# Kernel tuning notes

Hardware: AMD Instinct MI355X
Metric: run time of the kernel (lower is better)

Reference implementation:

```python
import jax, jax.numpy as jnp
import numpy as np

B, K, IN, CH, M, N = 1024, 64, 128, 256, 4, 16


def setup_inputs() -> dict:
    key = jax.random.key(0)
    ks = jax.random.split(key, 12)
    s = 0.02
    return {
        "user_node": jax.random.normal(ks[0], (B, K, IN), jnp.float32),
        "RIS_node": jax.random.normal(ks[1], (B, IN), jnp.float32),
        "cas_channel": jax.random.normal(ks[2], (B, K, 2 * M * N), jnp.float32),
        "d_link": jax.random.normal(ks[3], (B, K, 2 * M), jnp.float32),
        # f2_user: Linear(3*IN -> CH), ReLU, Linear(CH -> CH)
        "W1": jax.random.normal(ks[4], (3 * IN, CH), jnp.float32) * s,
        "b1": jnp.zeros((CH,), jnp.float32),
        "W2": jax.random.normal(ks[5], (CH, CH), jnp.float32) * s,
        "b2": jnp.zeros((CH,), jnp.float32),
        # f3_RIS: Linear(2*IN -> CH), ReLU, Linear(CH -> CH)
        "W3": jax.random.normal(ks[6], (2 * IN, CH), jnp.float32) * s,
        "b3": jnp.zeros((CH,), jnp.float32),
        "W4": jax.random.normal(ks[7], (CH, CH), jnp.float32) * s,
        "b4": jnp.zeros((CH,), jnp.float32),
    }


def _leave_one_out_max(x):
    # x: (B, K, D). Exact leave-one-out max via prefix/suffix cummax, O(K).
    prefix = jax.lax.cummax(x, axis=1)                      # max over 0..k
    suffix = jax.lax.cummax(x[:, ::-1], axis=1)[:, ::-1]    # max over k..K-1
    neg = jnp.full_like(x[:, :1], -jnp.inf)
    left = jnp.concatenate([neg, prefix[:, :-1]], axis=1)   # max over 0..k-1
    right = jnp.concatenate([suffix[:, 1:], neg], axis=1)   # max over k+1..K-1
    return jnp.maximum(left, right)


def reference(user_node, RIS_node, cas_channel, d_link,
              W1, b1, W2, b2, W3, b3, W4, b4):
    b, k, d = user_node.shape
    mean_user = jnp.mean(user_node, axis=1)                 # (B, IN)
    loo_max = _leave_one_out_max(user_node)                 # (B, K, IN)
    ris_b = jnp.broadcast_to(RIS_node[:, None, :], (b, k, d))
    feat = jnp.concatenate([user_node, loo_max, ris_b], axis=-1)  # (B, K, 3*IN)
    h_user = jax.nn.relu(feat @ W1 + b1) @ W2 + b2          # (B, K, CH)
    user_node_update = jnp.concatenate([user_node, h_user], axis=-1)  # (B,K,IN+CH)
    rfeat = jnp.concatenate([RIS_node, mean_user], axis=-1)  # (B, 2*IN)
    h_ris = jax.nn.relu(rfeat @ W3 + b3) @ W4 + b4          # (B, CH)
    RIS_node_update = jnp.concatenate([RIS_node, h_ris], axis=-1)    # (B, IN+CH)
    return user_node_update, RIS_node_update
```

## Files before the change

### kernel.cpp

```cpp
#include <hip/hip_runtime.h>

typedef __attribute__((ext_vector_type(8))) short short8;
typedef __attribute__((ext_vector_type(4))) float f32x4;
typedef __attribute__((ext_vector_type(2))) unsigned u32x2;

__device__ __forceinline__ unsigned short f2bf(float f) {
  unsigned u = __builtin_bit_cast(unsigned, f);
  u += 0x7fffu + ((u >> 16) & 1u);
  return (unsigned short)(u >> 16);
}
__device__ __forceinline__ float bf2f(unsigned short u) {
  return __builtin_bit_cast(float, (unsigned)u << 16);
}
__device__ __forceinline__ unsigned pkbf(float a, float b) {
  unsigned r;
  asm("v_cvt_pk_bf16_f32 %0, %1, %2" : "=v"(r) : "v"(a), "v"(b));
  return r;
}

__global__ __launch_bounds__(256) void wprep(
    const float* __restrict__ W1, const float* __restrict__ W2,
    const float* __restrict__ W3, const float* __restrict__ W4,
    unsigned short* __restrict__ W1f, unsigned short* __restrict__ W2f,
    unsigned short* __restrict__ W3f, unsigned short* __restrict__ W4f) {
  int idx = (blockIdx.x * 256 + threadIdx.x) * 4;
  const float* src; unsigned short* dst; int kb; int rel;
  if (idx < 98304)        { src = W1; dst = W1f; kb = 12; rel = idx; }
  else if (idx < 163840)  { src = W2; dst = W2f; kb = 8;  rel = idx - 98304; }
  else if (idx < 229376)  { src = W3; dst = W3f; kb = 8;  rel = idx - 163840; }
  else                    { src = W4; dst = W4f; kb = 8;  rel = idx - 229376; }
  int kk = rel >> 8, n0 = rel & 255;
  f32x4 t = *(const f32x4*)(src + rel);
  #pragma unroll
  for (int j = 0; j < 4; ++j) {
    int n = n0 + j;
    int lane = (n & 15) | (((kk >> 3) & 3) << 4);
    int di = (((n >> 4) * kb + (kk >> 5)) * 64 + lane) * 8 + (kk & 7);
    dst[di] = f2bf(t[j]);
  }
}

__global__ __launch_bounds__(512, 4) void fusedU(
    const float* __restrict__ user, const float* __restrict__ ris,
    const unsigned short* __restrict__ W1f, const unsigned short* __restrict__ W2f,
    const float* __restrict__ b1, const float* __restrict__ b2,
    float* __restrict__ out0, unsigned short* __restrict__ meanb) {
  __shared__ __align__(16) unsigned short smem[16896];
  unsigned short* const U    = smem;
  unsigned short* const Hb   = smem;
  unsigned short* const m1s  = smem + 16384;
  unsigned short* const m2s  = smem + 16512;
  unsigned short* const ams  = smem + 16640;
  unsigned short* const risl = smem + 16768;

  const int tid = threadIdx.x;
  const int bx = blockIdx.x;
  const size_t ubase = (size_t)bx * 8192;

  #pragma unroll
  for (int it = 0; it < 4; ++it) {
    int e = it * 2048 + tid * 4;
    f32x4 t = *(const f32x4*)(user + ubase + e);
    int row = e >> 7, col = e & 127;
    *(f32x4*)(out0 + (size_t)(bx * 64 + row) * 384 + col) = t;
    u32x2 p = { pkbf(t[0], t[1]), pkbf(t[2], t[3]) };
    int cc = col >> 3, sub = col & 7;
    *(u32x2*)(U + row * 128 + ((cc ^ (row & 7)) << 3) + sub) = p;
  }
  if (tid < 128) risl[tid] = f2bf(ris[bx * 128 + tid]);
  __syncthreads();

  const int lane = tid & 63, wn = tid >> 6;
  const int r = lane & 15;
  const int k8 = (lane >> 4) * 8;
  const int j4 = (lane >> 4) * 4;

  if (tid < 128) {
    int c = tid;
    int cc = c >> 3, sub = c & 7;
    float m1 = -3.402823466e38f, m2 = -3.402823466e38f, s = 0.f;
    int amx = 0;
    #pragma unroll 8
    for (int row = 0; row < 64; ++row) {
      float v = bf2f(U[row * 128 + ((cc ^ (row & 7)) << 3) + sub]);
      s += v;
      if (v > m1) { m2 = m1; m1 = v; amx = row; }
      else if (v > m2) { m2 = v; }
    }
    m1s[c] = f2bf(m1); m2s[c] = f2bf(m2); ams[c] = (unsigned short)amx;
    meanb[bx * 128 + c] = f2bf(s * (1.f / 64.f));
  }

  f32x4 acc[4][2];
  #pragma unroll
  for (int a = 0; a < 4; ++a) { acc[a][0] = (f32x4)0.f; acc[a][1] = (f32x4)0.f; }

  #pragma unroll
  for (int fs = 0; fs < 4; ++fs) {
    short8 af[4];
    #pragma unroll
    for (int mf = 0; mf < 4; ++mf) {
      int row = mf * 16 + r;
      int cc = fs * 4 + (lane >> 4);
      af[mf] = *(const short8*)(U + row * 128 + ((cc ^ (row & 7)) << 3));
    }
    short8 w0 = *(const short8*)&W1f[(size_t)(((wn * 2 + 0) * 12 + fs) * 64 + lane) * 8];
    short8 w1 = *(const short8*)&W1f[(size_t)(((wn * 2 + 1) * 12 + fs) * 64 + lane) * 8];
    #pragma unroll
    for (int mf = 0; mf < 4; ++mf) {
      acc[mf][0] = __builtin_amdgcn_mfma_f32_16x16x32_bf16(af[mf], w0, acc[mf][0], 0, 0, 0);
      acc[mf][1] = __builtin_amdgcn_mfma_f32_16x16x32_bf16(af[mf], w1, acc[mf][1], 0, 0, 0);
    }
  }
  #pragma unroll
  for (int fs = 0; fs < 4; ++fs) {
    short8 v = *(const short8*)(risl + fs * 32 + k8);
    short8 w0 = *(const short8*)&W1f[(size_t)(((wn * 2 + 0) * 12 + 8 + fs) * 64 + lane) * 8];
    short8 w1 = *(const short8*)&W1f[(size_t)(((wn * 2 + 1) * 12 + 8 + fs) * 64 + lane) * 8];
    #pragma unroll
    for (int mf = 0; mf < 4; ++mf) {
      acc[mf][0] = __builtin_amdgcn_mfma_f32_16x16x32_bf16(v, w0, acc[mf][0], 0, 0, 0);
      acc[mf][1] = __builtin_amdgcn_mfma_f32_16x16x32_bf16(v, w1, acc[mf][1], 0, 0, 0);
    }
  }
  __syncthreads();

  #pragma unroll
  for (int fs = 0; fs < 4; ++fs) {
    int c0 = fs * 32 + k8;
    short8 m1v = *(const short8*)(m1s + c0);
    short8 m2v = *(const short8*)(m2s + c0);
    short8 amv = *(const short8*)(ams + c0);
    short8 w0 = *(const short8*)&W1f[(size_t)(((wn * 2 + 0) * 12 + 4 + fs) * 64 + lane) * 8];
    short8 w1 = *(const short8*)&W1f[(size_t)(((wn * 2 + 1) * 12 + 4 + fs) * 64 + lane) * 8];
    #pragma unroll
    for (int mf = 0; mf < 4; ++mf) {
      int rr = mf * 16 + r;
      short8 t;
      #pragma unroll
      for (int j = 0; j < 8; ++j)
        t[j] = ((unsigned short)amv[j] == (unsigned short)rr) ? m2v[j] : m1v[j];
      acc[mf][0] = __builtin_amdgcn_mfma_f32_16x16x32_bf16(t, w0, acc[mf][0], 0, 0, 0);
      acc[mf][1] = __builtin_amdgcn_mfma_f32_16x16x32_bf16(t, w1, acc[mf][1], 0, 0, 0);
    }
  }

  float ba[2] = { b1[wn * 32 + r], b1[wn * 32 + 16 + r] };
  #pragma unroll
  for (int mf = 0; mf < 4; ++mf)
    #pragma unroll
    for (int nf = 0; nf < 2; ++nf)
      #pragma unroll
      for (int j = 0; j < 4; ++j) {
        int rr = mf * 16 + j4 + j;
        int col = wn * 32 + nf * 16 + r;
        int cc = col >> 3;
        Hb[rr * 256 + ((cc ^ (rr & 7)) << 3) + (col & 7)] =
            f2bf(fmaxf(acc[mf][nf][j] + ba[nf], 0.f));
      }
  __syncthreads();

  f32x4 acc2[4][2];
  #pragma unroll
  for (int a = 0; a < 4; ++a) { acc2[a][0] = (f32x4)0.f; acc2[a][1] = (f32x4)0.f; }
  #pragma unroll
  for (int kc = 0; kc < 8; ++kc) {
    short8 af[4];
    #pragma unroll
    for (int mf = 0; mf < 4; ++mf) {
      int rr = mf * 16 + r;
      int cc = kc * 4 + (lane >> 4);
      af[mf] = *(const short8*)(Hb + rr * 256 + ((cc ^ (rr & 7)) << 3));
    }
    short8 w0 = *(const short8*)&W2f[(size_t)(((wn * 2 + 0) * 8 + kc) * 64 + lane) * 8];
    short8 w1 = *(const short8*)&W2f[(size_t)(((wn * 2 + 1) * 8 + kc) * 64 + lane) * 8];
    #pragma unroll
    for (int mf = 0; mf < 4; ++mf) {
      acc2[mf][0] = __builtin_amdgcn_mfma_f32_16x16x32_bf16(af[mf], w0, acc2[mf][0], 0, 0, 0);
      acc2[mf][1] = __builtin_amdgcn_mfma_f32_16x16x32_bf16(af[mf], w1, acc2[mf][1], 0, 0, 0);
    }
  }

  float bb[2] = { b2[wn * 32 + r], b2[wn * 32 + 16 + r] };
  #pragma unroll
  for (int mf = 0; mf < 4; ++mf)
    #pragma unroll
    for (int nf = 0; nf < 2; ++nf)
      #pragma unroll
      for (int j = 0; j < 4; ++j) {
        int rr = mf * 16 + j4 + j;
        int col = wn * 32 + nf * 16 + r;
        out0[(size_t)(bx * 64 + rr) * 384 + 128 + col] = acc2[mf][nf][j] + bb[nf];
      }
}

__global__ __launch_bounds__(512, 4) void fusedR(
    const float* __restrict__ ris, const unsigned short* __restrict__ meanb,
    const unsigned short* __restrict__ W3f, const unsigned short* __restrict__ W4f,
    const float* __restrict__ b3, const float* __restrict__ b4,
    float* __restrict__ out1) {
  __shared__ unsigned short Hb[64 * 256];

  const int tid = threadIdx.x;
  const int row0 = blockIdx.x * 64;

  #pragma unroll
  for (int it = 0; it < 4; ++it) {
    int e = it * 2048 + tid * 4;
    f32x4 t = *(const f32x4*)(ris + (size_t)row0 * 128 + e);
    int row = e >> 7, col = e & 127;
    *(f32x4*)(out1 + (size_t)(row0 + row) * 384 + col) = t;
  }

  const int lane = tid & 63, wn = tid >> 6;
  const int r = lane & 15;
  const int k8 = (lane >> 4) * 8;
  const int j4 = (lane >> 4) * 4;

  f32x4 acc[4][2];
  #pragma unroll
  for (int a = 0; a < 4; ++a) { acc[a][0] = (f32x4)0.f; acc[a][1] = (f32x4)0.f; }

  #pragma unroll
  for (int fs = 0; fs < 8; ++fs) {
    short8 af[4];
    if (fs < 4) {
      #pragma unroll
      for (int mf = 0; mf < 4; ++mf) {
        const float* p = &ris[(size_t)(row0 + mf * 16 + r) * 128 + fs * 32 + k8];
        f32x4 t0 = *(const f32x4*)p;
        f32x4 t1 = *(const f32x4*)(p + 4);
        short8 t;
        #pragma unroll
        for (int j = 0; j < 4; ++j) { t[j] = (short)f2bf(t0[j]); t[4 + j] = (short)f2bf(t1[j]); }
        af[mf] = t;
      }
    } else {
      #pragma unroll
      for (int mf = 0; mf < 4; ++mf)
        af[mf] = *(const short8*)&meanb[(size_t)(row0 + mf * 16 + r) * 128 + (fs - 4) * 32 + k8];
    }
    short8 w0 = *(const short8*)&W3f[(size_t)(((wn * 2 + 0) * 8 + fs) * 64 + lane) * 8];
    short8 w1 = *(const short8*)&W3f[(size_t)(((wn * 2 + 1) * 8 + fs) * 64 + lane) * 8];
    #pragma unroll
    for (int mf = 0; mf < 4; ++mf) {
      acc[mf][0] = __builtin_amdgcn_mfma_f32_16x16x32_bf16(af[mf], w0, acc[mf][0], 0, 0, 0);
      acc[mf][1] = __builtin_amdgcn_mfma_f32_16x16x32_bf16(af[mf], w1, acc[mf][1], 0, 0, 0);
    }
  }

  float ba[2] = { b3[wn * 32 + r], b3[wn * 32 + 16 + r] };
  #pragma unroll
  for (int mf = 0; mf < 4; ++mf)
    #pragma unroll
    for (int nf = 0; nf < 2; ++nf)
      #pragma unroll
      for (int j = 0; j < 4; ++j) {
        int rr = mf * 16 + j4 + j;
        int col = wn * 32 + nf * 16 + r;
        int cc = col >> 3;
        Hb[rr * 256 + ((cc ^ (rr & 7)) << 3) + (col & 7)] =
            f2bf(fmaxf(acc[mf][nf][j] + ba[nf], 0.f));
      }
  __syncthreads();

  f32x4 acc2[4][2];
  #pragma unroll
  for (int a = 0; a < 4; ++a) { acc2[a][0] = (f32x4)0.f; acc2[a][1] = (f32x4)0.f; }
  #pragma unroll
  for (int kc = 0; kc < 8; ++kc) {
    short8 af[4];
    #pragma unroll
    for (int mf = 0; mf < 4; ++mf) {
      int rr = mf * 16 + r;
      int cc = kc * 4 + (lane >> 4);
      af[mf] = *(const short8*)(Hb + rr * 256 + ((cc ^ (rr & 7)) << 3));
    }
    short8 w0 = *(const short8*)&W4f[(size_t)(((wn * 2 + 0) * 8 + kc) * 64 + lane) * 8];
    short8 w1 = *(const short8*)&W4f[(size_t)(((wn * 2 + 1) * 8 + kc) * 64 + lane) * 8];
    #pragma unroll
    for (int mf = 0; mf < 4; ++mf) {
      acc2[mf][0] = __builtin_amdgcn_mfma_f32_16x16x32_bf16(af[mf], w0, acc2[mf][0], 0, 0, 0);
      acc2[mf][1] = __builtin_amdgcn_mfma_f32_16x16x32_bf16(af[mf], w1, acc2[mf][1], 0, 0, 0);
    }
  }

  float bb[2] = { b4[wn * 32 + r], b4[wn * 32 + 16 + r] };
  #pragma unroll
  for (int mf = 0; mf < 4; ++mf)
    #pragma unroll
    for (int nf = 0; nf < 2; ++nf)
      #pragma unroll
      for (int j = 0; j < 4; ++j) {
        int rr = mf * 16 + j4 + j;
        int col = wn * 32 + nf * 16 + r;
        out1[(size_t)(row0 + rr) * 384 + 128 + col] = acc2[mf][nf][j] + bb[nf];
      }
}

extern "C" void kernel_launch(void* const* d_in, const int* in_sizes, int n_in,
                              void* d_out, int out_size, void* d_ws, size_t ws_size,
                              hipStream_t stream) {
  const float* user = (const float*)d_in[0];
  const float* ris  = (const float*)d_in[1];
  const float* W1 = (const float*)d_in[4];
  const float* b1 = (const float*)d_in[5];
  const float* W2 = (const float*)d_in[6];
  const float* b2 = (const float*)d_in[7];
  const float* W3 = (const float*)d_in[8];
  const float* b3 = (const float*)d_in[9];
  const float* W4 = (const float*)d_in[10];
  const float* b4 = (const float*)d_in[11];

  float* out0 = (float*)d_out;
  float* out1 = out0 + (size_t)65536 * 384;

  char* ws = (char*)d_ws;
  unsigned short* meanb = (unsigned short*)(ws);
  unsigned short* W1f   = (unsigned short*)(ws + 262144);
  unsigned short* W2f   = (unsigned short*)(ws + 458752);
  unsigned short* W3f   = (unsigned short*)(ws + 589824);
  unsigned short* W4f   = (unsigned short*)(ws + 720896);

  hipLaunchKernelGGL(wprep, dim3(288), dim3(256), 0, stream,
                     W1, W2, W3, W4, W1f, W2f, W3f, W4f);
  hipLaunchKernelGGL(fusedU, dim3(1024), dim3(512), 0, stream,
                     user, ris, W1f, W2f, b1, b2, out0, meanb);
  hipLaunchKernelGGL(fusedR, dim3(16), dim3(512), 0, stream,
                     ris, meanb, W3f, W4f, b3, b4, out1);
}
```

Before: 70.64 us.

## Split passthrough copy into extra blocks and prefetch weight fragments in batches

Adds 512 extra blocks to the main kernel that only copy user_node into the first 128 columns of out0, taking that strided store off the compute blocks. The compute blocks now load W1/W2 fragments in batches of four k-steps ahead of the MFMA loops so global latency overlaps, and the mean store moves to the end. Launch bounds drop from 4 to 2 waves per SIMD to make room for the extra registers, which lowers occupancy.

```diff
diff --git a/kernel.cpp b/kernel.cpp
--- a/kernel.cpp
+++ b/kernel.cpp
@@ -40,11 +40,23 @@
   }
 }
 
-__global__ __launch_bounds__(512, 4) void fusedU(
+__global__ __launch_bounds__(512, 2) void mega(
     const float* __restrict__ user, const float* __restrict__ ris,
     const unsigned short* __restrict__ W1f, const unsigned short* __restrict__ W2f,
     const float* __restrict__ b1, const float* __restrict__ b2,
     float* __restrict__ out0, unsigned short* __restrict__ meanb) {
+  if (blockIdx.x >= 1024) {
+    int cb = blockIdx.x - 1024;
+    #pragma unroll
+    for (int it = 0; it < 8; ++it) {
+      int g = cb * 4096 + it * 512 + threadIdx.x;
+      f32x4 t = *((const f32x4*)user + g);
+      int row = g >> 5, col = (g & 31) << 2;
+      *(f32x4*)(out0 + (size_t)row * 384 + col) = t;
+    }
+    return;
+  }
+
   __shared__ __align__(16) unsigned short smem[16896];
   unsigned short* const U    = smem;
   unsigned short* const Hb   = smem;
@@ -62,7 +74,6 @@
     int e = it * 2048 + tid * 4;
     f32x4 t = *(const f32x4*)(user + ubase + e);
     int row = e >> 7, col = e & 127;
-    *(f32x4*)(out0 + (size_t)(bx * 64 + row) * 384 + col) = t;
     u32x2 p = { pkbf(t[0], t[1]), pkbf(t[2], t[3]) };
     int cc = col >> 3, sub = col & 7;
     *(u32x2*)(U + row * 128 + ((cc ^ (row & 7)) << 3) + sub) = p;
@@ -75,53 +86,72 @@
   const int k8 = (lane >> 4) * 8;
   const int j4 = (lane >> 4) * 4;
 
+  float my_s = 0.f;
   if (tid < 128) {
-    int c = tid;
-    int cc = c >> 3, sub = c & 7;
-    float m1 = -3.402823466e38f, m2 = -3.402823466e38f, s = 0.f;
+    int c = tid, cc = c >> 3, sub = c & 7;
+    float m1 = -3.402823466e38f, m2 = -3.402823466e38f;
     int amx = 0;
     #pragma unroll 8
     for (int row = 0; row < 64; ++row) {
       float v = bf2f(U[row * 128 + ((cc ^ (row & 7)) << 3) + sub]);
-      s += v;
+      my_s += v;
       if (v > m1) { m2 = m1; m1 = v; amx = row; }
       else if (v > m2) { m2 = v; }
     }
     m1s[c] = f2bf(m1); m2s[c] = f2bf(m2); ams[c] = (unsigned short)amx;
-    meanb[bx * 128 + c] = f2bf(s * (1.f / 64.f));
   }
 
   f32x4 acc[4][2];
   #pragma unroll
   for (int a = 0; a < 4; ++a) { acc[a][0] = (f32x4)0.f; acc[a][1] = (f32x4)0.f; }
 
+  {
+    short8 wv[4][2];
+    #pragma unroll
+    for (int fs = 0; fs < 4; ++fs) {
+      wv[fs][0] = *(const short8*)&W1f[(size_t)(((wn * 2 + 0) * 12 + fs) * 64 + lane) * 8];
+      wv[fs][1] = *(const short8*)&W1f[(size_t)(((wn * 2 + 1) * 12 + fs) * 64 + lane) * 8];
+    }
+    #pragma unroll
+    for (int fs = 0; fs < 4; ++fs) {
+      short8 af[4];
+      #pragma unroll
+      for (int mf = 0; mf < 4; ++mf) {
+        int row = mf * 16 + r;
+        int cc = fs * 4 + (lane >> 4);
+        af[mf] = *(const short8*)(U + row * 128 + ((cc ^ (row & 7)) << 3));
+      }
+      #pragma unroll
+      for (int mf = 0; mf < 4; ++mf) {
+        acc[mf][0] = __builtin_amdgcn_mfma_f32_16x16x32_bf16(af[mf], wv[fs][0], acc[mf][0], 0, 0, 0);
+        acc[mf][1] = __builtin_amdgcn_mfma_f32_16x16x32_bf16(af[mf], wv[fs][1], acc[mf][1], 0, 0, 0);
+      }
+    }
+  }
+
+  {
+    short8 wv[4][2];
+    #pragma unroll
+    for (int fs = 0; fs < 4; ++fs) {
+      wv[fs][0] = *(const short8*)&W1f[(size_t)(((wn * 2 + 0) * 12 + 8 + fs) * 64 + lane) * 8];
+      wv[fs][1] = *(const short8*)&W1f[(size_t)(((wn * 2 + 1) * 12 + 8 + fs) * 64 + lane) * 8];
+    }
+    #pragma unroll
+    for (int fs = 0; fs < 4; ++fs) {
+      short8 v = *(const short8*)(risl + fs * 32 + k8);
+      #pragma unroll
+      for (int mf = 0; mf < 4; ++mf) {
+        acc[mf][0] = __builtin_amdgcn_mfma_f32_16x16x32_bf16(v, wv[fs][0], acc[mf][0], 0, 0, 0);
+        acc[mf][1] = __builtin_amdgcn_mfma_f32_16x16x32_bf16(v, wv[fs][1], acc[mf][1], 0, 0, 0);
+      }
+    }
+  }
+
+  short8 wvl[4][2];
   #pragma unroll
   for (int fs = 0; fs < 4; ++fs) {
-    short8 af[4];
-    #pragma unroll
-    for (int mf = 0; mf < 4; ++mf) {
-      int row = mf * 16 + r;
-      int cc = fs * 4 + (lane >> 4);
-      af[mf] = *(const short8*)(U + row * 128 + ((cc ^ (row & 7)) << 3));
-    }
-    short8 w0 = *(const short8*)&W1f[(size_t)(((wn * 2 + 0) * 12 + fs) * 64 + lane) * 8];
-    short8 w1 = *(const short8*)&W1f[(size_t)(((wn * 2 + 1) * 12 + fs) * 64 + lane) * 8];
-    #pragma unroll
-    for (int mf = 0; mf < 4; ++mf) {
-      acc[mf][0] = __builtin_amdgcn_mfma_f32_16x16x32_bf16(af[mf], w0, acc[mf][0], 0, 0, 0);
-      acc[mf][1] = __builtin_amdgcn_mfma_f32_16x16x32_bf16(af[mf], w1, acc[mf][1], 0, 0, 0);
-    }
-  }
-  #pragma unroll
-  for (int fs = 0; fs < 4; ++fs) {
-    short8 v = *(const short8*)(risl + fs * 32 + k8);
-    short8 w0 = *(const short8*)&W1f[(size_t)(((wn * 2 + 0) * 12 + 8 + fs) * 64 + lane) * 8];
-    short8 w1 = *(const short8*)&W1f[(size_t)(((wn * 2 + 1) * 12 + 8 + fs) * 64 + lane) * 8];
-    #pragma unroll
-    for (int mf = 0; mf < 4; ++mf) {
-      acc[mf][0] = __builtin_amdgcn_mfma_f32_16x16x32_bf16(v, w0, acc[mf][0], 0, 0, 0);
-      acc[mf][1] = __builtin_amdgcn_mfma_f32_16x16x32_bf16(v, w1, acc[mf][1], 0, 0, 0);
-    }
+    wvl[fs][0] = *(const short8*)&W1f[(size_t)(((wn * 2 + 0) * 12 + 4 + fs) * 64 + lane) * 8];
+    wvl[fs][1] = *(const short8*)&W1f[(size_t)(((wn * 2 + 1) * 12 + 4 + fs) * 64 + lane) * 8];
   }
   __syncthreads();
 
@@ -131,8 +161,6 @@
     short8 m1v = *(const short8*)(m1s + c0);
     short8 m2v = *(const short8*)(m2s + c0);
     short8 amv = *(const short8*)(ams + c0);
-    short8 w0 = *(const short8*)&W1f[(size_t)(((wn * 2 + 0) * 12 + 4 + fs) * 64 + lane) * 8];
-    short8 w1 = *(const short8*)&W1f[(size_t)(((wn * 2 + 1) * 12 + 4 + fs) * 64 + lane) * 8];
     #pragma unroll
     for (int mf = 0; mf < 4; ++mf) {
       int rr = mf * 16 + r;
@@ -140,8 +168,8 @@
       #pragma unroll
       for (int j = 0; j < 8; ++j)
         t[j] = ((unsigned short)amv[j] == (unsigned short)rr) ? m2v[j] : m1v[j];
-      acc[mf][0] = __builtin_amdgcn_mfma_f32_16x16x32_bf16(t, w0, acc[mf][0], 0, 0, 0);
-      acc[mf][1] = __builtin_amdgcn_mfma_f32_16x16x32_bf16(t, w1, acc[mf][1], 0, 0, 0);
+      acc[mf][0] = __builtin_amdgcn_mfma_f32_16x16x32_bf16(t, wvl[fs][0], acc[mf][0], 0, 0, 0);
+      acc[mf][1] = __builtin_amdgcn_mfma_f32_16x16x32_bf16(t, wvl[fs][1], acc[mf][1], 0, 0, 0);
     }
   }
 
@@ -158,13 +186,20 @@
         Hb[rr * 256 + ((cc ^ (rr & 7)) << 3) + (col & 7)] =
             f2bf(fmaxf(acc[mf][nf][j] + ba[nf], 0.f));
       }
+
+  short8 wv2[4][2];
+  #pragma unroll
+  for (int kc = 0; kc < 4; ++kc) {
+    wv2[kc][0] = *(const short8*)&W2f[(size_t)(((wn * 2 + 0) * 8 + kc) * 64 + lane) * 8];
+    wv2[kc][1] = *(const short8*)&W2f[(size_t)(((wn * 2 + 1) * 8 + kc) * 64 + lane) * 8];
+  }
   __syncthreads();
 
   f32x4 acc2[4][2];
   #pragma unroll
   for (int a = 0; a < 4; ++a) { acc2[a][0] = (f32x4)0.f; acc2[a][1] = (f32x4)0.f; }
   #pragma unroll
-  for (int kc = 0; kc < 8; ++kc) {
+  for (int kc = 0; kc < 4; ++kc) {
     short8 af[4];
     #pragma unroll
     for (int mf = 0; mf < 4; ++mf) {
@@ -172,12 +207,33 @@
       int cc = kc * 4 + (lane >> 4);
       af[mf] = *(const short8*)(Hb + rr * 256 + ((cc ^ (rr & 7)) << 3));
     }
-    short8 w0 = *(const short8*)&W2f[(size_t)(((wn * 2 + 0) * 8 + kc) * 64 + lane) * 8];
-    short8 w1 = *(const short8*)&W2f[(size_t)(((wn * 2 + 1) * 8 + kc) * 64 + lane) * 8];
-    #pragma unroll
-    for (int mf = 0; mf < 4; ++mf) {
-      acc2[mf][0] = __builtin_amdgcn_mfma_f32_16x16x32_bf16(af[mf], w0, acc2[mf][0], 0, 0, 0);
-      acc2[mf][1] = __builtin_amdgcn_mfma_f32_16x16x32_bf16(af[mf], w1, acc2[mf][1], 0, 0, 0);
+    #pragma unroll
+    for (int mf = 0; mf < 4; ++mf) {
+      acc2[mf][0] = __builtin_amdgcn_mfma_f32_16x16x32_bf16(af[mf], wv2[kc][0], acc2[mf][0], 0, 0, 0);
+      acc2[mf][1] = __builtin_amdgcn_mfma_f32_16x16x32_bf16(af[mf], wv2[kc][1], acc2[mf][1], 0, 0, 0);
+    }
+  }
+  {
+    short8 wv[4][2];
+    #pragma unroll
+    for (int kc = 0; kc < 4; ++kc) {
+      wv[kc][0] = *(const short8*)&W2f[(size_t)(((wn * 2 + 0) * 8 + 4 + kc) * 64 + lane) * 8];
+      wv[kc][1] = *(const short8*)&W2f[(size_t)(((wn * 2 + 1) * 8 + 4 + kc) * 64 + lane) * 8];
+    }
+    #pragma unroll
+    for (int kc = 0; kc < 4; ++kc) {
+      short8 af[4];
+      #pragma unroll
+      for (int mf = 0; mf < 4; ++mf) {
+        int rr = mf * 16 + r;
+        int cc = (4 + kc) * 4 + (lane >> 4);
+        af[mf] = *(const short8*)(Hb + rr * 256 + ((cc ^ (rr & 7)) << 3));
+      }
+      #pragma unroll
+      for (int mf = 0; mf < 4; ++mf) {
+        acc2[mf][0] = __builtin_amdgcn_mfma_f32_16x16x32_bf16(af[mf], wv[kc][0], acc2[mf][0], 0, 0, 0);
+        acc2[mf][1] = __builtin_amdgcn_mfma_f32_16x16x32_bf16(af[mf], wv[kc][1], acc2[mf][1], 0, 0, 0);
+      }
     }
   }
 
@@ -192,6 +248,8 @@
         int col = wn * 32 + nf * 16 + r;
         out0[(size_t)(bx * 64 + rr) * 384 + 128 + col] = acc2[mf][nf][j] + bb[nf];
       }
+
+  if (tid < 128) meanb[bx * 128 + tid] = f2bf(my_s * (1.f / 64.f));
 }
 
 __global__ __launch_bounds__(512, 4) void fusedR(
@@ -324,7 +382,7 @@
 
   hipLaunchKernelGGL(wprep, dim3(288), dim3(256), 0, stream,
                      W1, W2, W3, W4, W1f, W2f, W3f, W4f);
-  hipLaunchKernelGGL(fusedU, dim3(1024), dim3(512), 0, stream,
+  hipLaunchKernelGGL(mega, dim3(1536), dim3(512), 0, stream,
                      user, ris, W1f, W2f, b1, b2, out0, meanb);
   hipLaunchKernelGGL(fusedR, dim3(16), dim3(512), 0, stream,
                      ris, meanb, W3f, W4f, b3, b4, out1);
```

Measured after the change: 73.48 us. +4.0%, slower.

## Halve fusedU block to 4 waves with 64-column per-wave tiles and MFMA priority

Applied to the files above, without the earlier changes.

The fusedU kernel now runs 256 threads (4 waves) per block instead of 512. Each wave computes a 64x64 output tile (4x4 MFMA fragments) instead of 64x32, so each A fragment loaded from LDS is reused across four B fragments. s_setprio is raised around the MFMA bursts, and the mean store is moved to the end of the kernel. This raises accumulator register pressure (launch bounds 256,3) and halves the threads available for the copy and reduction phases.

```diff
diff --git a/kernel.cpp b/kernel.cpp
--- a/kernel.cpp
+++ b/kernel.cpp
@@ -40,7 +40,7 @@
   }
 }
 
-__global__ __launch_bounds__(512, 4) void fusedU(
+__global__ __launch_bounds__(256, 3) void fusedU(
     const float* __restrict__ user, const float* __restrict__ ris,
     const unsigned short* __restrict__ W1f, const unsigned short* __restrict__ W2f,
     const float* __restrict__ b1, const float* __restrict__ b2,
@@ -58,8 +58,8 @@
   const size_t ubase = (size_t)bx * 8192;
 
   #pragma unroll
-  for (int it = 0; it < 4; ++it) {
-    int e = it * 2048 + tid * 4;
+  for (int it = 0; it < 8; ++it) {
+    int e = it * 1024 + tid * 4;
     f32x4 t = *(const f32x4*)(user + ubase + e);
     int row = e >> 7, col = e & 127;
     *(f32x4*)(out0 + (size_t)(bx * 64 + row) * 384 + col) = t;
@@ -72,56 +72,66 @@
 
   const int lane = tid & 63, wn = tid >> 6;
   const int r = lane & 15;
-  const int k8 = (lane >> 4) * 8;
-  const int j4 = (lane >> 4) * 4;
-
+  const int g = lane >> 4;
+  const int k8 = g * 8;
+  const int j4 = g * 4;
+
+  float my_s = 0.f;
   if (tid < 128) {
-    int c = tid;
-    int cc = c >> 3, sub = c & 7;
-    float m1 = -3.402823466e38f, m2 = -3.402823466e38f, s = 0.f;
+    int c = tid, cc = c >> 3, sub = c & 7;
+    float m1 = -3.402823466e38f, m2 = -3.402823466e38f;
     int amx = 0;
     #pragma unroll 8
     for (int row = 0; row < 64; ++row) {
       float v = bf2f(U[row * 128 + ((cc ^ (row & 7)) << 3) + sub]);
-      s += v;
+      my_s += v;
       if (v > m1) { m2 = m1; m1 = v; amx = row; }
       else if (v > m2) { m2 = v; }
     }
     m1s[c] = f2bf(m1); m2s[c] = f2bf(m2); ams[c] = (unsigned short)amx;
-    meanb[bx * 128 + c] = f2bf(s * (1.f / 64.f));
-  }
-
-  f32x4 acc[4][2];
-  #pragma unroll
-  for (int a = 0; a < 4; ++a) { acc[a][0] = (f32x4)0.f; acc[a][1] = (f32x4)0.f; }
+  }
+
+  f32x4 acc[4][4];
+  #pragma unroll
+  for (int a = 0; a < 4; ++a)
+    #pragma unroll
+    for (int q = 0; q < 4; ++q) acc[a][q] = (f32x4)0.f;
 
   #pragma unroll
   for (int fs = 0; fs < 4; ++fs) {
-    short8 af[4];
+    short8 af[4], bf[4];
     #pragma unroll
     for (int mf = 0; mf < 4; ++mf) {
       int row = mf * 16 + r;
-      int cc = fs * 4 + (lane >> 4);
+      int cc = fs * 4 + g;
       af[mf] = *(const short8*)(U + row * 128 + ((cc ^ (row & 7)) << 3));
     }
-    short8 w0 = *(const short8*)&W1f[(size_t)(((wn * 2 + 0) * 12 + fs) * 64 + lane) * 8];
-    short8 w1 = *(const short8*)&W1f[(size_t)(((wn * 2 + 1) * 12 + fs) * 64 + lane) * 8];
-    #pragma unroll
-    for (int mf = 0; mf < 4; ++mf) {
-      acc[mf][0] = __builtin_amdgcn_mfma_f32_16x16x32_bf16(af[mf], w0, acc[mf][0], 0, 0, 0);
-      acc[mf][1] = __builtin_amdgcn_mfma_f32_16x16x32_bf16(af[mf], w1, acc[mf][1], 0, 0, 0);
-    }
-  }
+    #pragma unroll
+    for (int nf = 0; nf < 4; ++nf)
+      bf[nf] = *(const short8*)&W1f[(size_t)(((wn * 4 + nf) * 12 + fs) * 64 + lane) * 8];
+    __builtin_amdgcn_s_setprio(1);
+    #pragma unroll
+    for (int mf = 0; mf < 4; ++mf)
+      #pragma unroll
+      for (int nf = 0; nf < 4; ++nf)
+        acc[mf][nf] = __builtin_amdgcn_mfma_f32_16x16x32_bf16(af[mf], bf[nf], acc[mf][nf], 0, 0, 0);
+    __builtin_amdgcn_s_setprio(0);
+  }
+
   #pragma unroll
   for (int fs = 0; fs < 4; ++fs) {
     short8 v = *(const short8*)(risl + fs * 32 + k8);
-    short8 w0 = *(const short8*)&W1f[(size_t)(((wn * 2 + 0) * 12 + 8 + fs) * 64 + lane) * 8];
-    short8 w1 = *(const short8*)&W1f[(size_t)(((wn * 2 + 1) * 12 + 8 + fs) * 64 + lane) * 8];
-    #pragma unroll
-    for (int mf = 0; mf < 4; ++mf) {
-      acc[mf][0] = __builtin_amdgcn_mfma_f32_16x16x32_bf16(v, w0, acc[mf][0], 0, 0, 0);
-      acc[mf][1] = __builtin_amdgcn_mfma_f32_16x16x32_bf16(v, w1, acc[mf][1], 0, 0, 0);
-    }
+    short8 bf[4];
+    #pragma unroll
+    for (int nf = 0; nf < 4; ++nf)
+      bf[nf] = *(const short8*)&W1f[(size_t)(((wn * 4 + nf) * 12 + 8 + fs) * 64 + lane) * 8];
+    __builtin_amdgcn_s_setprio(1);
+    #pragma unroll
+    for (int mf = 0; mf < 4; ++mf)
+      #pragma unroll
+      for (int nf = 0; nf < 4; ++nf)
+        acc[mf][nf] = __builtin_amdgcn_mfma_f32_16x16x32_bf16(v, bf[nf], acc[mf][nf], 0, 0, 0);
+    __builtin_amdgcn_s_setprio(0);
   }
   __syncthreads();
 
@@ -131,8 +141,11 @@
     short8 m1v = *(const short8*)(m1s + c0);
     short8 m2v = *(const short8*)(m2s + c0);
     short8 amv = *(const short8*)(ams + c0);
-    short8 w0 = *(const short8*)&W1f[(size_t)(((wn * 2 + 0) * 12 + 4 + fs) * 64 + lane) * 8];
-    short8 w1 = *(const short8*)&W1f[(size_t)(((wn * 2 + 1) * 12 + 4 + fs) * 64 + lane) * 8];
+    short8 bf[4];
+    #pragma unroll
+    for (int nf = 0; nf < 4; ++nf)
+      bf[nf] = *(const short8*)&W1f[(size_t)(((wn * 4 + nf) * 12 + 4 + fs) * 64 + lane) * 8];
+    __builtin_amdgcn_s_setprio(1);
     #pragma unroll
     for (int mf = 0; mf < 4; ++mf) {
       int rr = mf * 16 + r;
@@ -140,58 +153,71 @@
       #pragma unroll
       for (int j = 0; j < 8; ++j)
         t[j] = ((unsigned short)amv[j] == (unsigned short)rr) ? m2v[j] : m1v[j];
-      acc[mf][0] = __builtin_amdgcn_mfma_f32_16x16x32_bf16(t, w0, acc[mf][0], 0, 0, 0);
-      acc[mf][1] = __builtin_amdgcn_mfma_f32_16x16x32_bf16(t, w1, acc[mf][1], 0, 0, 0);
-    }
-  }
-
-  float ba[2] = { b1[wn * 32 + r], b1[wn * 32 + 16 + r] };
+      #pragma unroll
+      for (int nf = 0; nf < 4; ++nf)
+        acc[mf][nf] = __builtin_amdgcn_mfma_f32_16x16x32_bf16(t, bf[nf], acc[mf][nf], 0, 0, 0);
+    }
+    __builtin_amdgcn_s_setprio(0);
+  }
+
+  float ba[4];
+  #pragma unroll
+  for (int nf = 0; nf < 4; ++nf) ba[nf] = b1[wn * 64 + nf * 16 + r];
   #pragma unroll
   for (int mf = 0; mf < 4; ++mf)
     #pragma unroll
-    for (int nf = 0; nf < 2; ++nf)
+    for (int nf = 0; nf < 4; ++nf)
       #pragma unroll
       for (int j = 0; j < 4; ++j) {
         int rr = mf * 16 + j4 + j;
-        int col = wn * 32 + nf * 16 + r;
+        int col = wn * 64 + nf * 16 + r;
         int cc = col >> 3;
         Hb[rr * 256 + ((cc ^ (rr & 7)) << 3) + (col & 7)] =
             f2bf(fmaxf(acc[mf][nf][j] + ba[nf], 0.f));
       }
   __syncthreads();
 
-  f32x4 acc2[4][2];
-  #pragma unroll
-  for (int a = 0; a < 4; ++a) { acc2[a][0] = (f32x4)0.f; acc2[a][1] = (f32x4)0.f; }
+  f32x4 acc2[4][4];
+  #pragma unroll
+  for (int a = 0; a < 4; ++a)
+    #pragma unroll
+    for (int q = 0; q < 4; ++q) acc2[a][q] = (f32x4)0.f;
   #pragma unroll
   for (int kc = 0; kc < 8; ++kc) {
-    short8 af[4];
+    short8 af[4], bf[4];
     #pragma unroll
     for (int mf = 0; mf < 4; ++mf) {
       int rr = mf * 16 + r;
-      int cc = kc * 4 + (lane >> 4);
+      int cc = kc * 4 + g;
       af[mf] = *(const short8*)(Hb + rr * 256 + ((cc ^ (rr & 7)) << 3));
     }
-    short8 w0 = *(const short8*)&W2f[(size_t)(((wn * 2 + 0) * 8 + kc) * 64 + lane) * 8];
-    short8 w1 = *(const short8*)&W2f[(size_t)(((wn * 2 + 1) * 8 + kc) * 64 + lane) * 8];
-    #pragma unroll
-    for (int mf = 0; mf < 4; ++mf) {
-      acc2[mf][0] = __builtin_amdgcn_mfma_f32_16x16x32_bf16(af[mf], w0, acc2[mf][0], 0, 0, 0);
-      acc2[mf][1] = __builtin_amdgcn_mfma_f32_16x16x32_bf16(af[mf], w1, acc2[mf][1], 0, 0, 0);
-    }
-  }
-
-  float bb[2] = { b2[wn * 32 + r], b2[wn * 32 + 16 + r] };
+    #pragma unroll
+    for (int nf = 0; nf < 4; ++nf)
+      bf[nf] = *(const short8*)&W2f[(size_t)(((wn * 4 + nf) * 8 + kc) * 64 + lane) * 8];
+    __builtin_amdgcn_s_setprio(1);
+    #pragma unroll
+    for (int mf = 0; mf < 4; ++mf)
+      #pragma unroll
+      for (int nf = 0; nf < 4; ++nf)
+        acc2[mf][nf] = __builtin_amdgcn_mfma_f32_16x16x32_bf16(af[mf], bf[nf], acc2[mf][nf], 0, 0, 0);
+    __builtin_amdgcn_s_setprio(0);
+  }
+
+  float bb[4];
+  #pragma unroll
+  for (int nf = 0; nf < 4; ++nf) bb[nf] = b2[wn * 64 + nf * 16 + r];
   #pragma unroll
   for (int mf = 0; mf < 4; ++mf)
     #pragma unroll
-    for (int nf = 0; nf < 2; ++nf)
+    for (int nf = 0; nf < 4; ++nf)
       #pragma unroll
       for (int j = 0; j < 4; ++j) {
         int rr = mf * 16 + j4 + j;
-        int col = wn * 32 + nf * 16 + r;
+        int col = wn * 64 + nf * 16 + r;
         out0[(size_t)(bx * 64 + rr) * 384 + 128 + col] = acc2[mf][nf][j] + bb[nf];
       }
+
+  if (tid < 128) meanb[bx * 128 + tid] = f2bf(my_s * (1.f / 64.f));
 }
 
 __global__ __launch_bounds__(512, 4) void fusedR(
@@ -324,7 +350,7 @@
 
   hipLaunchKernelGGL(wprep, dim3(288), dim3(256), 0, stream,
                      W1, W2, W3, W4, W1f, W2f, W3f, W4f);
-  hipLaunchKernelGGL(fusedU, dim3(1024), dim3(512), 0, stream,
+  hipLaunchKernelGGL(fusedU, dim3(1024), dim3(256), 0, stream,
                      user, ris, W1f, W2f, b1, b2, out0, meanb);
   hipLaunchKernelGGL(fusedR, dim3(16), dim3(512), 0, stream,
                      ris, meanb, W3f, W4f, b3, b4, out1);
```

Measured after the change: 73.17 us. 1.04x slower.

## Process two batch items per fusedU block to reuse weight fragments

Applied to the files above, without the earlier changes.

Each fusedU block now handles two batch items (128 rows) instead of one, so every W1/W2 fragment loaded from global memory feeds 8 MFMA row tiles instead of 4. The grid is halved, LDS per block doubles, and accumulators double, with launch bounds relaxed to one block per CU. The cost is higher register pressure and lower occupancy, which may reduce latency hiding, plus fewer blocks for load balancing across CUs.

```diff
diff --git a/kernel.cpp b/kernel.cpp
--- a/kernel.cpp
+++ b/kernel.cpp
@@ -40,85 +40,91 @@
   }
 }
 
-__global__ __launch_bounds__(512, 4) void fusedU(
+__global__ __launch_bounds__(512, 1) void fusedU(
     const float* __restrict__ user, const float* __restrict__ ris,
     const unsigned short* __restrict__ W1f, const unsigned short* __restrict__ W2f,
     const float* __restrict__ b1, const float* __restrict__ b2,
     float* __restrict__ out0, unsigned short* __restrict__ meanb) {
-  __shared__ __align__(16) unsigned short smem[16896];
+  __shared__ __align__(16) unsigned short smem[33792];
   unsigned short* const U    = smem;
   unsigned short* const Hb   = smem;
-  unsigned short* const m1s  = smem + 16384;
-  unsigned short* const m2s  = smem + 16512;
-  unsigned short* const ams  = smem + 16640;
-  unsigned short* const risl = smem + 16768;
+  unsigned short* const m1s  = smem + 32768;
+  unsigned short* const m2s  = smem + 33024;
+  unsigned short* const ams  = smem + 33280;
+  unsigned short* const risl = smem + 33536;
 
   const int tid = threadIdx.x;
   const int bx = blockIdx.x;
-  const size_t ubase = (size_t)bx * 8192;
-
-  #pragma unroll
-  for (int it = 0; it < 4; ++it) {
+  const size_t ubase = (size_t)bx * 16384;
+
+  #pragma unroll
+  for (int it = 0; it < 8; ++it) {
     int e = it * 2048 + tid * 4;
     f32x4 t = *(const f32x4*)(user + ubase + e);
     int row = e >> 7, col = e & 127;
-    *(f32x4*)(out0 + (size_t)(bx * 64 + row) * 384 + col) = t;
+    *(f32x4*)(out0 + (size_t)(bx * 128 + row) * 384 + col) = t;
     u32x2 p = { pkbf(t[0], t[1]), pkbf(t[2], t[3]) };
     int cc = col >> 3, sub = col & 7;
     *(u32x2*)(U + row * 128 + ((cc ^ (row & 7)) << 3) + sub) = p;
   }
-  if (tid < 128) risl[tid] = f2bf(ris[bx * 128 + tid]);
+  if (tid < 256) risl[tid] = f2bf(ris[bx * 256 + tid]);
   __syncthreads();
 
   const int lane = tid & 63, wn = tid >> 6;
-  const int r = lane & 15;
-  const int k8 = (lane >> 4) * 8;
-  const int j4 = (lane >> 4) * 4;
-
-  if (tid < 128) {
-    int c = tid;
+  const int r = lane & 15, g = lane >> 4;
+  const int k8 = g * 8;
+  const int j4 = g * 4;
+
+  float my_s = 0.f;
+  if (tid < 256) {
+    int bh = tid >> 7, c = tid & 127;
     int cc = c >> 3, sub = c & 7;
-    float m1 = -3.402823466e38f, m2 = -3.402823466e38f, s = 0.f;
+    float m1 = -3.402823466e38f, m2 = -3.402823466e38f;
     int amx = 0;
     #pragma unroll 8
     for (int row = 0; row < 64; ++row) {
-      float v = bf2f(U[row * 128 + ((cc ^ (row & 7)) << 3) + sub]);
-      s += v;
+      int gr = bh * 64 + row;
+      float v = bf2f(U[gr * 128 + ((cc ^ (gr & 7)) << 3) + sub]);
+      my_s += v;
       if (v > m1) { m2 = m1; m1 = v; amx = row; }
       else if (v > m2) { m2 = v; }
     }
-    m1s[c] = f2bf(m1); m2s[c] = f2bf(m2); ams[c] = (unsigned short)amx;
-    meanb[bx * 128 + c] = f2bf(s * (1.f / 64.f));
-  }
-
-  f32x4 acc[4][2];
-  #pragma unroll
-  for (int a = 0; a < 4; ++a) { acc[a][0] = (f32x4)0.f; acc[a][1] = (f32x4)0.f; }
+    m1s[bh * 128 + c] = f2bf(m1);
+    m2s[bh * 128 + c] = f2bf(m2);
+    ams[bh * 128 + c] = (unsigned short)amx;
+  }
+
+  f32x4 acc[8][2];
+  #pragma unroll
+  for (int a = 0; a < 8; ++a) { acc[a][0] = (f32x4)0.f; acc[a][1] = (f32x4)0.f; }
 
   #pragma unroll
   for (int fs = 0; fs < 4; ++fs) {
-    short8 af[4];
-    #pragma unroll
-    for (int mf = 0; mf < 4; ++mf) {
-      int row = mf * 16 + r;
-      int cc = fs * 4 + (lane >> 4);
-      af[mf] = *(const short8*)(U + row * 128 + ((cc ^ (row & 7)) << 3));
-    }
     short8 w0 = *(const short8*)&W1f[(size_t)(((wn * 2 + 0) * 12 + fs) * 64 + lane) * 8];
     short8 w1 = *(const short8*)&W1f[(size_t)(((wn * 2 + 1) * 12 + fs) * 64 + lane) * 8];
-    #pragma unroll
-    for (int mf = 0; mf < 4; ++mf) {
+    short8 af[8];
+    #pragma unroll
+    for (int mf = 0; mf < 8; ++mf) {
+      int row = mf * 16 + r;
+      int cc = fs * 4 + g;
+      af[mf] = *(const short8*)(U + row * 128 + ((cc ^ (row & 7)) << 3));
+    }
+    #pragma unroll
+    for (int mf = 0; mf < 8; ++mf) {
       acc[mf][0] = __builtin_amdgcn_mfma_f32_16x16x32_bf16(af[mf], w0, acc[mf][0], 0, 0, 0);
       acc[mf][1] = __builtin_amdgcn_mfma_f32_16x16x32_bf16(af[mf], w1, acc[mf][1], 0, 0, 0);
     }
   }
+
   #pragma unroll
   for (int fs = 0; fs < 4; ++fs) {
-    short8 v = *(const short8*)(risl + fs * 32 + k8);
     short8 w0 = *(const short8*)&W1f[(size_t)(((wn * 2 + 0) * 12 + 8 + fs) * 64 + lane) * 8];
     short8 w1 = *(const short8*)&W1f[(size_t)(((wn * 2 + 1) * 12 + 8 + fs) * 64 + lane) * 8];
-    #pragma unroll
-    for (int mf = 0; mf < 4; ++mf) {
+    short8 v0 = *(const short8*)(risl + fs * 32 + k8);
+    short8 v1 = *(const short8*)(risl + 128 + fs * 32 + k8);
+    #pragma unroll
+    for (int mf = 0; mf < 8; ++mf) {
+      const short8 v = (mf < 4) ? v0 : v1;
       acc[mf][0] = __builtin_amdgcn_mfma_f32_16x16x32_bf16(v, w0, acc[mf][0], 0, 0, 0);
       acc[mf][1] = __builtin_amdgcn_mfma_f32_16x16x32_bf16(v, w1, acc[mf][1], 0, 0, 0);
     }
@@ -127,19 +133,25 @@
 
   #pragma unroll
   for (int fs = 0; fs < 4; ++fs) {
-    int c0 = fs * 32 + k8;
-    short8 m1v = *(const short8*)(m1s + c0);
-    short8 m2v = *(const short8*)(m2s + c0);
-    short8 amv = *(const short8*)(ams + c0);
     short8 w0 = *(const short8*)&W1f[(size_t)(((wn * 2 + 0) * 12 + 4 + fs) * 64 + lane) * 8];
     short8 w1 = *(const short8*)&W1f[(size_t)(((wn * 2 + 1) * 12 + 4 + fs) * 64 + lane) * 8];
-    #pragma unroll
-    for (int mf = 0; mf < 4; ++mf) {
-      int rr = mf * 16 + r;
+    int c0 = fs * 32 + k8;
+    short8 m1a = *(const short8*)(m1s + c0);
+    short8 m2a = *(const short8*)(m2s + c0);
+    short8 ama = *(const short8*)(ams + c0);
+    short8 m1b_ = *(const short8*)(m1s + 128 + c0);
+    short8 m2b_ = *(const short8*)(m2s + 128 + c0);
+    short8 amb = *(const short8*)(ams + 128 + c0);
+    #pragma unroll
+    for (int mf = 0; mf < 8; ++mf) {
+      int rk = (mf * 16 + r) & 63;
+      const short8 m1v = (mf < 4) ? m1a : m1b_;
+      const short8 m2v = (mf < 4) ? m2a : m2b_;
+      const short8 amv = (mf < 4) ? ama : amb;
       short8 t;
       #pragma unroll
       for (int j = 0; j < 8; ++j)
-        t[j] = ((unsigned short)amv[j] == (unsigned short)rr) ? m2v[j] : m1v[j];
+        t[j] = ((unsigned short)amv[j] == (unsigned short)rk) ? m2v[j] : m1v[j];
       acc[mf][0] = __builtin_amdgcn_mfma_f32_16x16x32_bf16(t, w0, acc[mf][0], 0, 0, 0);
       acc[mf][1] = __builtin_amdgcn_mfma_f32_16x16x32_bf16(t, w1, acc[mf][1], 0, 0, 0);
     }
@@ -147,7 +159,7 @@
 
   float ba[2] = { b1[wn * 32 + r], b1[wn * 32 + 16 + r] };
   #pragma unroll
-  for (int mf = 0; mf < 4; ++mf)
+  for (int mf = 0; mf < 8; ++mf)
     #pragma unroll
     for (int nf = 0; nf < 2; ++nf)
       #pragma unroll
@@ -160,22 +172,22 @@
       }
   __syncthreads();
 
-  f32x4 acc2[4][2];
-  #pragma unroll
-  for (int a = 0; a < 4; ++a) { acc2[a][0] = (f32x4)0.f; acc2[a][1] = (f32x4)0.f; }
+  f32x4 acc2[8][2];
+  #pragma unroll
+  for (int a = 0; a < 8; ++a) { acc2[a][0] = (f32x4)0.f; acc2[a][1] = (f32x4)0.f; }
   #pragma unroll
   for (int kc = 0; kc < 8; ++kc) {
-    short8 af[4];
-    #pragma unroll
-    for (int mf = 0; mf < 4; ++mf) {
-      int rr = mf * 16 + r;
-      int cc = kc * 4 + (lane >> 4);
-      af[mf] = *(const short8*)(Hb + rr * 256 + ((cc ^ (rr & 7)) << 3));
-    }
     short8 w0 = *(const short8*)&W2f[(size_t)(((wn * 2 + 0) * 8 + kc) * 64 + lane) * 8];
     short8 w1 = *(const short8*)&W2f[(size_t)(((wn * 2 + 1) * 8 + kc) * 64 + lane) * 8];
-    #pragma unroll
-    for (int mf = 0; mf < 4; ++mf) {
+    short8 af[8];
+    #pragma unroll
+    for (int mf = 0; mf < 8; ++mf) {
+      int rr = mf * 16 + r;
+      int cc = kc * 4 + g;
+      af[mf] = *(const short8*)(Hb + rr * 256 + ((cc ^ (rr & 7)) << 3));
+    }
+    #pragma unroll
+    for (int mf = 0; mf < 8; ++mf) {
       acc2[mf][0] = __builtin_amdgcn_mfma_f32_16x16x32_bf16(af[mf], w0, acc2[mf][0], 0, 0, 0);
       acc2[mf][1] = __builtin_amdgcn_mfma_f32_16x16x32_bf16(af[mf], w1, acc2[mf][1], 0, 0, 0);
     }
@@ -183,15 +195,17 @@
 
   float bb[2] = { b2[wn * 32 + r], b2[wn * 32 + 16 + r] };
   #pragma unroll
-  for (int mf = 0; mf < 4; ++mf)
+  for (int mf = 0; mf < 8; ++mf)
     #pragma unroll
     for (int nf = 0; nf < 2; ++nf)
       #pragma unroll
       for (int j = 0; j < 4; ++j) {
         int rr = mf * 16 + j4 + j;
         int col = wn * 32 + nf * 16 + r;
-        out0[(size_t)(bx * 64 + rr) * 384 + 128 + col] = acc2[mf][nf][j] + bb[nf];
-      }
+        out0[(size_t)(bx * 128 + rr) * 384 + 128 + col] = acc2[mf][nf][j] + bb[nf];
+      }
+
+  if (tid < 256) meanb[bx * 256 + tid] = f2bf(my_s * (1.f / 64.f));
 }
 
 __global__ __launch_bounds__(512, 4) void fusedR(
@@ -324,7 +338,7 @@
 
   hipLaunchKernelGGL(wprep, dim3(288), dim3(256), 0, stream,
                      W1, W2, W3, W4, W1f, W2f, W3f, W4f);
-  hipLaunchKernelGGL(fusedU, dim3(1024), dim3(512), 0, stream,
+  hipLaunchKernelGGL(fusedU, dim3(512), dim3(512), 0, stream,
                      user, ris, W1f, W2f, b1, b2, out0, meanb);
   hipLaunchKernelGGL(fusedR, dim3(16), dim3(512), 0, stream,
                      ris, meanb, W3f, W4f, b3, b4, out1);
```

Result: slower. 81.99 us (+16.1%).
